# Optimization experiments

Measured on AMD Instinct MI355X. Metric: run time of the kernel, lower is better.

## Reference

```python
import jax, jax.numpy as jnp
import numpy as np

NUM_HEADS = 32
NUM_KV_HEADS = 8
HEAD_DIM = 128
ROPE_THETA = 10000.0


def _rope_cos_sin(seq_len, head_dim, dtype):
    # [seq, head_dim/2] angles, duplicated to [seq, head_dim] via concat (rotate-half convention)
    inv_freq = 1.0 / (ROPE_THETA ** (jnp.arange(0, head_dim, 2, dtype=jnp.float32) / head_dim))
    ang = jnp.arange(seq_len, dtype=jnp.float32)[:, None] * inv_freq[None, :]
    ang = jnp.concatenate([ang, ang], axis=-1)
    return jnp.cos(ang).astype(dtype), jnp.sin(ang).astype(dtype)


def _rotate_half(x):
    d = x.shape[-1] // 2
    return jnp.concatenate([-x[..., d:], x[..., :d]], axis=-1)


def setup_inputs() -> dict:
    key = jax.random.key(0)
    ks = jax.random.split(key, 5)
    E = NUM_HEADS * HEAD_DIM
    KVE = NUM_KV_HEADS * HEAD_DIM
    B, S = 2, 2048
    sc_in = 1.0 / np.sqrt(E)
    return {
        "x": jax.random.normal(ks[0], (B, S, E), jnp.float32),
        "Wq": jax.random.normal(ks[1], (E, E), jnp.float32) * sc_in,
        "Wk": jax.random.normal(ks[2], (E, KVE), jnp.float32) * sc_in,
        "Wv": jax.random.normal(ks[3], (E, KVE), jnp.float32) * sc_in,
        "Wo": jax.random.normal(ks[4], (E, E), jnp.float32) * sc_in,
    }


def reference(x, Wq, Wk, Wv, Wo):
    b, s, e = x.shape
    H, KV, D = NUM_HEADS, NUM_KV_HEADS, HEAD_DIM
    G = H // KV
    scale = 1.0 / np.sqrt(D)

    q = (x @ Wq).reshape(b, s, H, D).transpose(0, 2, 1, 3)    # [b,H,s,D]
    k = (x @ Wk).reshape(b, s, KV, D).transpose(0, 2, 1, 3)   # [b,KV,s,D]
    v = (x @ Wv).reshape(b, s, KV, D).transpose(0, 2, 1, 3)   # [b,KV,s,D]

    cos, sin = _rope_cos_sin(s, D, q.dtype)                   # [s,D]
    q = q * cos + _rotate_half(q) * sin
    k = k * cos + _rotate_half(k) * sin

    # GQA: group q heads by kv head instead of repeat_interleaving k/v
    qg = q.reshape(b, KV, G, s, D)
    attn = jnp.einsum("bkgqd,bkvd->bkgqv", qg, k) * scale     # [b,KV,G,s,s]

    causal = jnp.where(
        jnp.arange(s)[:, None] >= jnp.arange(s)[None, :], 0.0, -jnp.inf
    ).astype(jnp.float32)
    attn = attn.astype(jnp.float32) + causal
    attn = jax.nn.softmax(attn, axis=-1).astype(q.dtype)

    out = jnp.einsum("bkgqv,bkvd->bkgqd", attn, v)            # [b,KV,G,s,D]
    out = out.reshape(b, H, s, D).transpose(0, 2, 1, 3).reshape(b, s, H * D)
    return out @ Wo
```

## Files before the change

kernel.cpp:

```cpp
#include <hip/hip_runtime.h>
#include <stdint.h>
#include <math.h>

typedef short bf16x8 __attribute__((ext_vector_type(8)));
typedef float f32x4 __attribute__((ext_vector_type(4)));

#if __has_builtin(__builtin_amdgcn_exp2f)
#define EXP2F(x) __builtin_amdgcn_exp2f(x)
#else
#define EXP2F(x) exp2f(x)
#endif

static constexpr int Bn   = 2;
static constexpr int Sn   = 2048;
static constexpr int NH   = 32;
static constexpr int NKV  = 8;
static constexpr int Dh   = 128;
static constexpr int En   = NH * Dh;
static constexpr int KVEn = NKV * Dh;
static constexpr int QKVE = En + 2 * KVEn;
static constexpr int MT   = Bn * Sn;
static constexpr int QT   = Sn / 128;

__device__ __forceinline__ unsigned short f2bf(float f) {
  unsigned int u = __float_as_uint(f);
  u += 0x7FFFu + ((u >> 16) & 1u);
  return (unsigned short)(u >> 16);
}
__device__ __forceinline__ float bf2f(unsigned short h) {
  return __uint_as_float(((unsigned int)h) << 16);
}

typedef __attribute__((address_space(1))) void* gas_t;
typedef __attribute__((address_space(3))) void* las_t;
__device__ __forceinline__ void gl_lds16(const void* g, void* l) {
  __builtin_amdgcn_global_load_lds((gas_t)(uintptr_t)g, (las_t)(uint32_t)(uintptr_t)l,
                                   16, 0, 0);
}

#define VMW(n)  asm volatile("s_waitcnt vmcnt(" #n ")" ::: "memory")
#define LGKM0   asm volatile("s_waitcnt lgkmcnt(0)" ::: "memory")
#define SCHEDB  __builtin_amdgcn_sched_barrier(0)
#define BAR     __builtin_amdgcn_s_barrier()


__global__ void cast_bf16_kernel(const float* __restrict__ x,
                                 unsigned short* __restrict__ y, int n4) {
  int i = blockIdx.x * 256 + threadIdx.x;
  if (i >= n4) return;
  float4 v = ((const float4*)x)[i];
  ushort4 o;
  o.x = f2bf(v.x); o.y = f2bf(v.y); o.z = f2bf(v.z); o.w = f2bf(v.w);
  ((ushort4*)y)[i] = o;
}

__global__ void tcast_kernel(const float* __restrict__ W,
                             unsigned short* __restrict__ WT, int R, int C) {
  __shared__ float t[64][69];
  int tx = threadIdx.x & 15, ty = threadIdx.x >> 4;
  int r0 = blockIdx.y * 64, c0 = blockIdx.x * 64;
#pragma unroll
  for (int i = 0; i < 4; ++i) {
    float4 v = *(const float4*)&W[(size_t)(r0 + ty * 4 + i) * C + (c0 + tx * 4)];
    t[ty * 4 + i][tx * 4 + 0] = v.x;
    t[ty * 4 + i][tx * 4 + 1] = v.y;
    t[ty * 4 + i][tx * 4 + 2] = v.z;
    t[ty * 4 + i][tx * 4 + 3] = v.w;
  }
  __syncthreads();
#pragma unroll
  for (int i = 0; i < 4; ++i) {
    ushort4 o;
    o.x = f2bf(t[tx * 4 + 0][ty * 4 + i]);
    o.y = f2bf(t[tx * 4 + 1][ty * 4 + i]);
    o.z = f2bf(t[tx * 4 + 2][ty * 4 + i]);
    o.w = f2bf(t[tx * 4 + 3][ty * 4 + i]);
    *(ushort4*)&WT[(size_t)(c0 + ty * 4 + i) * R + (r0 + tx * 4)] = o;
  }
}

__global__ void rope_table_kernel(float2* __restrict__ cs) {
  int i = blockIdx.x * 256 + threadIdx.x;
  int s = i >> 6, d = i & 63;
  float inv = powf(10000.0f, -(float)d * (1.0f / 64.0f));
  float a = (float)s * inv;
  cs[i] = make_float2(cosf(a), sinf(a));
}

__global__ void rope_kernel(unsigned short* __restrict__ q,
                            const float2* __restrict__ cs, int rowstride, float scl) {
  int row = blockIdx.x;
  int s = row & (Sn - 1);
  int h = threadIdx.x >> 3, d0 = (threadIdx.x & 7) * 8;
  size_t base = (size_t)row * rowstride + (size_t)h * Dh + d0;
  bf16x8 lo = *(const bf16x8*)&q[base];
  bf16x8 hi = *(const bf16x8*)&q[base + 64];
  bf16x8 olo, ohi;
#pragma unroll
  for (int e = 0; e < 8; ++e) {
    float2 c = cs[s * 64 + d0 + e];
    float x0 = bf2f((unsigned short)lo[e]);
    float x1 = bf2f((unsigned short)hi[e]);
    olo[e] = (short)f2bf((x0 * c.x - x1 * c.y) * scl);
    ohi[e] = (short)f2bf((x1 * c.x + x0 * c.y) * scl);
  }
  *(bf16x8*)&q[base] = olo;
  *(bf16x8*)&q[base + 64] = ohi;
}

__global__ void vtrans_kernel(const unsigned short* __restrict__ V, int rowstride,
                              unsigned short* __restrict__ Vt) {
  __shared__ unsigned short t[32][33];
  int bk = blockIdx.z;
  int b = bk >> 3, kv = bk & 7;
  int d = blockIdx.x * 32 + threadIdx.x;
  int s = blockIdx.y * 32 + threadIdx.y;
  t[threadIdx.y][threadIdx.x] = V[(size_t)(b * Sn + s) * rowstride + kv * Dh + d];
  __syncthreads();
  int dd = blockIdx.x * 32 + threadIdx.y;
  int so = blockIdx.y * 32 + threadIdx.x;
  Vt[((size_t)bk * Dh + dd) * Sn + so] = t[threadIdx.x][threadIdx.y];
}


__global__ __launch_bounds__(512, 2) void gemm256_kernel(
    const unsigned short* __restrict__ A, const unsigned short* __restrict__ BT,
    void* __restrict__ Cout, int M, int N, int K, int out_f32) {
  __shared__ unsigned short lds[2][4][128 * 64];
  const int tid = threadIdx.x;
  const int lane = tid & 63, wave = tid >> 6;
  const int r15 = lane & 15, kg = lane >> 4;
  const int wr = wave >> 2, wc = wave & 3;
  const int m0 = blockIdx.y * 256, n0 = blockIdx.x * 256;
  const char* Ab = (const char*)A;
  const char* Bb = (const char*)BT;
  const int KT = K >> 6;

  f32x4 acc[2][2][4][2] = {};
  bf16x8 ar[4][2];
  bf16x8 br[2][2][2];

#define STAGE_H(SRC, ROW0, KT_, SLOT)                                         \
  do {                                                                        \
    _Pragma("unroll") for (int ld = 0; ld < 2; ++ld) {                        \
      int _f = (ld * 512 + tid) * 16;                                         \
      int _row = _f >> 7, _cb = _f & 127;                                     \
      gl_lds16(SRC + ((size_t)((ROW0) + _row) * K + (size_t)(KT_) * 64) * 2 + \
                   (_cb ^ ((_row & 7) << 4)),                                 \
               (char*)(SLOT) + _f);                                           \
    }                                                                         \
  } while (0)

#define GPHASE(MH, NH, BUF, DO_LDA, DO_LDB, STAGE_STMT, WAIT_STMT)            \
  do {                                                                        \
    if (DO_LDA) {                                                             \
      const char* _as = (const char*)lds[BUF][MH];                            \
      _Pragma("unroll") for (int mf = 0; mf < 4; ++mf) {                      \
        int _r = wr * 64 + mf * 16 + r15;                                     \
        int _sw = (_r & 7) << 4;                                              \
        ar[mf][0] = *(const bf16x8*)(_as + _r * 128 + ((kg * 16) ^ _sw));     \
        ar[mf][1] = *(const bf16x8*)(_as + _r * 128 + ((64 + kg * 16) ^ _sw));\
      }                                                                       \
    }                                                                         \
    if (DO_LDB) {                                                             \
      const char* _bs = (const char*)lds[BUF][2 + NH];                        \
      _Pragma("unroll") for (int nf = 0; nf < 2; ++nf) {                      \
        int _r = wc * 32 + nf * 16 + r15;                                     \
        int _sw = (_r & 7) << 4;                                              \
        br[NH][nf][0] =                                                       \
            *(const bf16x8*)(_bs + _r * 128 + ((kg * 16) ^ _sw));             \
        br[NH][nf][1] =                                                       \
            *(const bf16x8*)(_bs + _r * 128 + ((64 + kg * 16) ^ _sw));        \
      }                                                                       \
    }                                                                         \
    STAGE_STMT;                                                               \
    if ((DO_LDA) || (DO_LDB)) { LGKM0; }                                      \
    SCHEDB;                                                                   \
    __builtin_amdgcn_s_setprio(1);                                            \
    _Pragma("unroll") for (int mf = 0; mf < 4; ++mf)                          \
      _Pragma("unroll") for (int n2 = 0; n2 < 2; ++n2) {                      \
        acc[MH][NH][mf][n2] = __builtin_amdgcn_mfma_f32_16x16x32_bf16(        \
            ar[mf][0], br[NH][n2][0], acc[MH][NH][mf][n2], 0, 0, 0);          \
        acc[MH][NH][mf][n2] = __builtin_amdgcn_mfma_f32_16x16x32_bf16(        \
            ar[mf][1], br[NH][n2][1], acc[MH][NH][mf][n2], 0, 0, 0);          \
      }                                                                       \
    __builtin_amdgcn_s_setprio(0);                                            \
    SCHEDB;                                                                   \
    WAIT_STMT;                                                                \
    BAR;                                                                      \
    SCHEDB;                                                                   \
  } while (0)

  STAGE_H(Ab, m0,       0, lds[0][0]);
  STAGE_H(Bb, n0,       0, lds[0][2]);
  STAGE_H(Ab, m0 + 128, 0, lds[0][1]);
  STAGE_H(Bb, n0 + 128, 0, lds[0][3]);
  STAGE_H(Ab, m0,       1, lds[1][0]);
  STAGE_H(Bb, n0,       1, lds[1][2]);
  VMW(8);
  SCHEDB;
  BAR;
  SCHEDB;

  for (int k = 0; k + 2 < KT; k += 2) {
    GPHASE(0, 0, 0, true,  true,  STAGE_H(Ab, m0 + 128, k + 1, lds[1][1]), VMW(6));
    GPHASE(0, 1, 0, false, true,  STAGE_H(Bb, n0 + 128, k + 1, lds[1][3]), VMW(10));
    GPHASE(1, 0, 0, true,  false, STAGE_H(Ab, m0,       k + 2, lds[0][0]), (void)0);
    GPHASE(1, 1, 0, false, false, STAGE_H(Bb, n0,       k + 2, lds[0][2]), VMW(8));
    GPHASE(0, 0, 1, true,  true,  STAGE_H(Ab, m0 + 128, k + 2, lds[0][1]), VMW(6));
    GPHASE(0, 1, 1, false, true,  STAGE_H(Bb, n0 + 128, k + 2, lds[0][3]), VMW(10));
    GPHASE(1, 0, 1, true,  false, STAGE_H(Ab, m0,       k + 3, lds[1][0]), (void)0);
    GPHASE(1, 1, 1, false, false, STAGE_H(Bb, n0,       k + 3, lds[1][2]), VMW(8));
  }
  GPHASE(0, 0, 0, true,  true,  STAGE_H(Ab, m0 + 128, KT - 1, lds[1][1]), VMW(6));
  GPHASE(0, 1, 0, false, true,  STAGE_H(Bb, n0 + 128, KT - 1, lds[1][3]), VMW(10));
  GPHASE(1, 0, 0, true,  false, (void)0, (void)0);
  GPHASE(1, 1, 0, false, false, (void)0, VMW(0));
  GPHASE(0, 0, 1, true,  true,  (void)0, (void)0);
  GPHASE(0, 1, 1, false, true,  (void)0, (void)0);
  GPHASE(1, 0, 1, true,  false, (void)0, (void)0);
  GPHASE(1, 1, 1, false, false, (void)0, (void)0);

#undef GPHASE
#undef STAGE_H

#pragma unroll
  for (int mh = 0; mh < 2; ++mh)
#pragma unroll
    for (int nh = 0; nh < 2; ++nh)
#pragma unroll
      for (int mf = 0; mf < 4; ++mf)
#pragma unroll
        for (int nf = 0; nf < 2; ++nf)
#pragma unroll
          for (int t = 0; t < 4; ++t) {
            int row = m0 + mh * 128 + wr * 64 + mf * 16 + kg * 4 + t;
            int col = n0 + nh * 128 + wc * 32 + nf * 16 + r15;
            if (out_f32)
              ((float*)Cout)[(size_t)row * N + col] = acc[mh][nh][mf][nf][t];
            else
              ((unsigned short*)Cout)[(size_t)row * N + col] =
                  f2bf(acc[mh][nh][mf][nf][t]);
          }
}


__device__ __forceinline__ void sm_update(f32x4 sc[4], f32x4 o[8],
                                          float mrow[4], float lrow[4],
                                          bool diag, int qrow0, int kt,
                                          int r15, int kg, char* Pw) {
  if (diag) {
#pragma unroll
    for (int kf = 0; kf < 4; ++kf) {
      int kvg = kt * 64 + kf * 16 + r15;
#pragma unroll
      for (int t = 0; t < 4; ++t)
        if (kvg > qrow0 + kg * 4 + t) sc[kf][t] = -1e30f;
    }
  }
  float nm[4];
  bool grow = false;
#pragma unroll
  for (int t = 0; t < 4; ++t) {
    float v = fmaxf(fmaxf(sc[0][t], sc[1][t]), fmaxf(sc[2][t], sc[3][t]));
#pragma unroll
    for (int off = 1; off < 16; off <<= 1) v = fmaxf(v, __shfl_xor(v, off, 16));
    nm[t] = v;
    grow = grow || (v > mrow[t] + 8.0f);
  }
  if (__any(grow)) {
#pragma unroll
    for (int t = 0; t < 4; ++t) {
      float mx = fmaxf(mrow[t], nm[t]);
      float sm = EXP2F(mrow[t] - mx);
      mrow[t] = mx;
      lrow[t] *= sm;
#pragma unroll
      for (int nf = 0; nf < 8; ++nf) o[nf][t] *= sm;
    }
  }
#pragma unroll
  for (int kf = 0; kf < 4; ++kf)
#pragma unroll
    for (int t = 0; t < 4; ++t) sc[kf][t] = EXP2F(sc[kf][t] - mrow[t]);
#pragma unroll
  for (int t = 0; t < 4; ++t) {
    float v = sc[0][t] + sc[1][t] + sc[2][t] + sc[3][t];
#pragma unroll
    for (int off = 1; off < 16; off <<= 1) v += __shfl_xor(v, off, 16);
    lrow[t] += v;
  }
#pragma unroll
  for (int kf = 0; kf < 4; ++kf)
#pragma unroll
    for (int t = 0; t < 4; ++t) {
      int r = kg * 4 + t, c = kf * 16 + r15;
      *(unsigned short*)(Pw + r * 128 + ((c * 2) ^ ((r & 7) << 4))) = f2bf(sc[kf][t]);
    }
}

__global__ __launch_bounds__(512, 4) void attn_kernel(
    const unsigned short* __restrict__ Q, const unsigned short* __restrict__ Kl,
    const unsigned short* __restrict__ Vt, unsigned short* __restrict__ AO) {
  __shared__ unsigned short Ks[2][64 * 128];
  __shared__ unsigned short Vs[2][128 * 64];
  __shared__ unsigned short Ps[8][16 * 64];
  const int tid = threadIdx.x, lane = tid & 63, wave = tid >> 6;
  const int h = blockIdx.x, b = blockIdx.z;
  const int qt = (QT - 1) - blockIdx.y;
  const int kvh = h >> 2;
  const int r15 = lane & 15, kg = lane >> 4;
  const int qrow0 = qt * 128 + wave * 16;
  const int kmax = 2 * qt + 2;

  bf16x8 qf[4];
#pragma unroll
  for (int db = 0; db < 4; ++db)
    qf[db] = *(const bf16x8*)&Q[(size_t)(b * Sn + qrow0 + r15) * QKVE +
                                h * Dh + db * 32 + kg * 8];

  f32x4 o[8] = {};
  float mrow[4] = {-1e30f, -1e30f, -1e30f, -1e30f};
  float lrow[4] = {0.f, 0.f, 0.f, 0.f};

  const char* Kbase = (const char*)Kl + (size_t)(b * Sn) * (QKVE * 2) + kvh * 256;
  const char* Vbase = (const char*)Vt + (size_t)((b * NKV + kvh) * Dh) * (Sn * 2);

  auto stage = [&](int kt, int bi) {
#pragma unroll
    for (int c = 0; c < 2; ++c) {
      int f = (c * 512 + tid) * 16;
      int row = f >> 8, cb = f & 255;
      gl_lds16(Kbase + (size_t)(kt * 64 + row) * (QKVE * 2) + (cb ^ ((row & 7) << 4)),
               (char*)Ks[bi] + f);
    }
#pragma unroll
    for (int c = 0; c < 2; ++c) {
      int f = (c * 512 + tid) * 16;
      int row = f >> 7, cb = f & 127;
      gl_lds16(Vbase + (size_t)row * (Sn * 2) + kt * 128 + (cb ^ ((row & 7) << 4)),
               (char*)Vs[bi] + f);
    }
  };

  stage(0, 0);
  __syncthreads();

  for (int kt = 0; kt < kmax; ++kt) {
    const int cur = kt & 1;
    if (kt + 1 < kmax) stage(kt + 1, cur ^ 1);
    if (kt * 64 <= qrow0 + 15) {
      const char* Kc = (const char*)Ks[cur];
      const char* Vc = (const char*)Vs[cur];
      f32x4 sc[4] = {};
      __builtin_amdgcn_s_setprio(1);
#pragma unroll
      for (int db = 0; db < 4; ++db) {
#pragma unroll
        for (int kf = 0; kf < 4; ++kf) {
          int krow = kf * 16 + r15;
          int cb = (db * 32 + kg * 8) * 2;
          bf16x8 kb = *(const bf16x8*)(Kc + krow * 256 + (cb ^ ((krow & 7) << 4)));
          sc[kf] = __builtin_amdgcn_mfma_f32_16x16x32_bf16(qf[db], kb, sc[kf], 0, 0, 0);
        }
      }
      __builtin_amdgcn_s_setprio(0);

      char* Pw = (char*)Ps[wave];
      bool diag = (kt * 64 + 63) > qrow0;
      sm_update(sc, o, mrow, lrow, diag, qrow0, kt, r15, kg, Pw);

      __builtin_amdgcn_s_setprio(1);
#pragma unroll
      for (int ks = 0; ks < 2; ++ks) {
        bf16x8 pa = *(const bf16x8*)(Pw + r15 * 128 + ((kg * 16 + ks * 64) ^ ((r15 & 7) << 4)));
#pragma unroll
        for (int nf = 0; nf < 8; ++nf) {
          int vrow = nf * 16 + r15;
          int cb = (ks * 32 + kg * 8) * 2;
          bf16x8 vb = *(const bf16x8*)(Vc + vrow * 128 + (cb ^ ((vrow & 7) << 4)));
          o[nf] = __builtin_amdgcn_mfma_f32_16x16x32_bf16(pa, vb, o[nf], 0, 0, 0);
        }
      }
      __builtin_amdgcn_s_setprio(0);
    }
    __syncthreads();
  }

  float rinv[4];
#pragma unroll
  for (int t = 0; t < 4; ++t) rinv[t] = 1.0f / lrow[t];
#pragma unroll
  for (int nf = 0; nf < 8; ++nf)
#pragma unroll
    for (int t = 0; t < 4; ++t) {
      int srow = qrow0 + kg * 4 + t;
      AO[(size_t)(b * Sn + srow) * En + h * Dh + nf * 16 + r15] = f2bf(o[nf][t] * rinv[t]);
    }
}


extern "C" void kernel_launch(void* const* d_in, const int* in_sizes, int n_in,
                              void* d_out, int out_size, void* d_ws, size_t ws_size,
                              hipStream_t stream) {
  const float* x  = (const float*)d_in[0];
  const float* Wq = (const float*)d_in[1];
  const float* Wk = (const float*)d_in[2];
  const float* Wv = (const float*)d_in[3];
  const float* Wo = (const float*)d_in[4];

  char* ws = (char*)d_ws;
  size_t off = 0;
  auto alloc = [&](size_t bytes) -> char* {
    char* p = ws + off;
    off += (bytes + 255) & ~(size_t)255;
    return p;
  };
  unsigned short* xb   = (unsigned short*)alloc((size_t)MT * En * 2);
  unsigned short* Wqkv = (unsigned short*)alloc((size_t)QKVE * En * 2);
  unsigned short* WoT  = (unsigned short*)alloc((size_t)En * En * 2);
  unsigned short* Cqkv = (unsigned short*)alloc((size_t)MT * QKVE * 2);
  unsigned short* Vt   = (unsigned short*)alloc((size_t)MT * KVEn * 2);
  float2* cs           = (float2*)alloc((size_t)Sn * 64 * sizeof(float2));
  unsigned short* AO   = xb;

  cast_bf16_kernel<<<MT * (En / 4) / 256, 256, 0, stream>>>(x, xb, MT * En / 4);
  tcast_kernel<<<dim3(En / 64, En / 64), 256, 0, stream>>>(Wq, Wqkv, En, En);
  tcast_kernel<<<dim3(KVEn / 64, En / 64), 256, 0, stream>>>(
      Wk, Wqkv + (size_t)En * En, En, KVEn);
  tcast_kernel<<<dim3(KVEn / 64, En / 64), 256, 0, stream>>>(
      Wv, Wqkv + (size_t)(En + KVEn) * En, En, KVEn);
  tcast_kernel<<<dim3(En / 64, En / 64), 256, 0, stream>>>(Wo, WoT, En, En);
  rope_table_kernel<<<Sn * 64 / 256, 256, 0, stream>>>(cs);

  gemm256_kernel<<<dim3(QKVE / 256, MT / 256), 512, 0, stream>>>(
      xb, Wqkv, Cqkv, MT, QKVE, En, 0);

  const float scl = 0.08838834764831845f * 1.4426950408889634f;
  rope_kernel<<<MT, 256, 0, stream>>>(Cqkv, cs, QKVE, scl);
  rope_kernel<<<MT, 64, 0, stream>>>(Cqkv + En, cs, QKVE, 1.0f);
  vtrans_kernel<<<dim3(Dh / 32, Sn / 32, Bn * NKV), dim3(32, 32), 0, stream>>>(
      Cqkv + En + KVEn, QKVE, Vt);

  attn_kernel<<<dim3(NH, QT, Bn), 512, 0, stream>>>(Cqkv, Cqkv + En, Vt, AO);

  gemm256_kernel<<<dim3(En / 256, MT / 256), 512, 0, stream>>>(
      AO, WoT, d_out, MT, En, En, 1);
}
```

Baseline: 555.0 us.

## Process two GQA query heads per attention block to reuse staged K/V tiles

Each attention block now handles two query heads that share the same KV head. Every K/V tile staged into shared memory feeds both heads, which halves global K/V traffic and the number of blocks launched. The cost is double the per-thread accumulator and Q-fragment registers, which may lower occupancy under the launch bounds of 512 threads and 4 blocks per CU, and fewer blocks means less parallelism for the causal load imbalance.

```diff
diff --git a/kernel.cpp b/kernel.cpp
--- a/kernel.cpp
+++ b/kernel.cpp
@@ -306,22 +306,25 @@
   __shared__ unsigned short Vs[2][128 * 64];
   __shared__ unsigned short Ps[8][16 * 64];
   const int tid = threadIdx.x, lane = tid & 63, wave = tid >> 6;
-  const int h = blockIdx.x, b = blockIdx.z;
+  const int h0 = blockIdx.x * 2, b = blockIdx.z;
   const int qt = (QT - 1) - blockIdx.y;
-  const int kvh = h >> 2;
+  const int kvh = h0 >> 2;
   const int r15 = lane & 15, kg = lane >> 4;
   const int qrow0 = qt * 128 + wave * 16;
   const int kmax = 2 * qt + 2;
 
-  bf16x8 qf[4];
-#pragma unroll
-  for (int db = 0; db < 4; ++db)
-    qf[db] = *(const bf16x8*)&Q[(size_t)(b * Sn + qrow0 + r15) * QKVE +
-                                h * Dh + db * 32 + kg * 8];
-
-  f32x4 o[8] = {};
-  float mrow[4] = {-1e30f, -1e30f, -1e30f, -1e30f};
-  float lrow[4] = {0.f, 0.f, 0.f, 0.f};
+  bf16x8 qf[2][4];
+#pragma unroll
+  for (int e = 0; e < 2; ++e)
+#pragma unroll
+    for (int db = 0; db < 4; ++db)
+      qf[e][db] = *(const bf16x8*)&Q[(size_t)(b * Sn + qrow0 + r15) * QKVE +
+                                     (h0 + e) * Dh + db * 32 + kg * 8];
+
+  f32x4 o[2][8] = {};
+  float mrow[2][4] = {{-1e30f, -1e30f, -1e30f, -1e30f},
+                      {-1e30f, -1e30f, -1e30f, -1e30f}};
+  float lrow[2][4] = {{0.f, 0.f, 0.f, 0.f}, {0.f, 0.f, 0.f, 0.f}};
 
   const char* Kbase = (const char*)Kl + (size_t)(b * Sn) * (QKVE * 2) + kvh * 256;
   const char* Vbase = (const char*)Vt + (size_t)((b * NKV + kvh) * Dh) * (Sn * 2);
@@ -352,51 +355,61 @@
     if (kt * 64 <= qrow0 + 15) {
       const char* Kc = (const char*)Ks[cur];
       const char* Vc = (const char*)Vs[cur];
-      f32x4 sc[4] = {};
-      __builtin_amdgcn_s_setprio(1);
-#pragma unroll
-      for (int db = 0; db < 4; ++db) {
-#pragma unroll
-        for (int kf = 0; kf < 4; ++kf) {
-          int krow = kf * 16 + r15;
-          int cb = (db * 32 + kg * 8) * 2;
-          bf16x8 kb = *(const bf16x8*)(Kc + krow * 256 + (cb ^ ((krow & 7) << 4)));
-          sc[kf] = __builtin_amdgcn_mfma_f32_16x16x32_bf16(qf[db], kb, sc[kf], 0, 0, 0);
-        }
-      }
-      __builtin_amdgcn_s_setprio(0);
-
       char* Pw = (char*)Ps[wave];
       bool diag = (kt * 64 + 63) > qrow0;
-      sm_update(sc, o, mrow, lrow, diag, qrow0, kt, r15, kg, Pw);
-
-      __builtin_amdgcn_s_setprio(1);
-#pragma unroll
-      for (int ks = 0; ks < 2; ++ks) {
-        bf16x8 pa = *(const bf16x8*)(Pw + r15 * 128 + ((kg * 16 + ks * 64) ^ ((r15 & 7) << 4)));
-#pragma unroll
-        for (int nf = 0; nf < 8; ++nf) {
-          int vrow = nf * 16 + r15;
-          int cb = (ks * 32 + kg * 8) * 2;
-          bf16x8 vb = *(const bf16x8*)(Vc + vrow * 128 + (cb ^ ((vrow & 7) << 4)));
-          o[nf] = __builtin_amdgcn_mfma_f32_16x16x32_bf16(pa, vb, o[nf], 0, 0, 0);
+#pragma unroll
+      for (int e = 0; e < 2; ++e) {
+        f32x4 sc[4] = {};
+        __builtin_amdgcn_s_setprio(1);
+#pragma unroll
+        for (int db = 0; db < 4; ++db) {
+#pragma unroll
+          for (int kf = 0; kf < 4; ++kf) {
+            int krow = kf * 16 + r15;
+            int cb = (db * 32 + kg * 8) * 2;
+            bf16x8 kb = *(const bf16x8*)(Kc + krow * 256 + (cb ^ ((krow & 7) << 4)));
+            sc[kf] = __builtin_amdgcn_mfma_f32_16x16x32_bf16(qf[e][db], kb, sc[kf],
+                                                             0, 0, 0);
+          }
         }
+        __builtin_amdgcn_s_setprio(0);
+
+        sm_update(sc, o[e], mrow[e], lrow[e], diag, qrow0, kt, r15, kg, Pw);
+
+        __builtin_amdgcn_s_setprio(1);
+#pragma unroll
+        for (int ks = 0; ks < 2; ++ks) {
+          bf16x8 pa = *(const bf16x8*)(Pw + r15 * 128 +
+                                       ((kg * 16 + ks * 64) ^ ((r15 & 7) << 4)));
+#pragma unroll
+          for (int nf = 0; nf < 8; ++nf) {
+            int vrow = nf * 16 + r15;
+            int cb = (ks * 32 + kg * 8) * 2;
+            bf16x8 vb = *(const bf16x8*)(Vc + vrow * 128 + (cb ^ ((vrow & 7) << 4)));
+            o[e][nf] = __builtin_amdgcn_mfma_f32_16x16x32_bf16(pa, vb, o[e][nf],
+                                                               0, 0, 0);
+          }
+        }
+        __builtin_amdgcn_s_setprio(0);
       }
-      __builtin_amdgcn_s_setprio(0);
     }
     __syncthreads();
   }
 
-  float rinv[4];
-#pragma unroll
-  for (int t = 0; t < 4; ++t) rinv[t] = 1.0f / lrow[t];
-#pragma unroll
-  for (int nf = 0; nf < 8; ++nf)
-#pragma unroll
-    for (int t = 0; t < 4; ++t) {
-      int srow = qrow0 + kg * 4 + t;
-      AO[(size_t)(b * Sn + srow) * En + h * Dh + nf * 16 + r15] = f2bf(o[nf][t] * rinv[t]);
-    }
+#pragma unroll
+  for (int e = 0; e < 2; ++e) {
+    float rinv[4];
+#pragma unroll
+    for (int t = 0; t < 4; ++t) rinv[t] = 1.0f / lrow[e][t];
+#pragma unroll
+    for (int nf = 0; nf < 8; ++nf)
+#pragma unroll
+      for (int t = 0; t < 4; ++t) {
+        int srow = qrow0 + kg * 4 + t;
+        AO[(size_t)(b * Sn + srow) * En + (h0 + e) * Dh + nf * 16 + r15] =
+            f2bf(o[e][nf][t] * rinv[t]);
+      }
+  }
 }
 
 
@@ -442,7 +455,7 @@
   vtrans_kernel<<<dim3(Dh / 32, Sn / 32, Bn * NKV), dim3(32, 32), 0, stream>>>(
       Cqkv + En + KVEn, QKVE, Vt);
 
-  attn_kernel<<<dim3(NH, QT, Bn), 512, 0, stream>>>(Cqkv, Cqkv + En, Vt, AO);
+  attn_kernel<<<dim3(NH / 2, QT, Bn), 512, 0, stream>>>(Cqkv, Cqkv + En, Vt, AO);
 
   gemm256_kernel<<<dim3(En / 256, MT / 256), 512, 0, stream>>>(
       AO, WoT, d_out, MT, En, En, 1);
```

Result: slower. 920.0 us (+65.8%).
